# Kernel optimization log

Measured on AMD Instinct MI355X. Metric: run time of the kernel, lower is better.

## Reference

```python
import jax, jax.numpy as jnp
import numpy as np

B, T, C = 8, 2048, 1024
NEG = -1e30  # stand-in for -inf in the stable-softmax running max


def setup_inputs() -> dict:
    key = jax.random.key(0)
    ks = jax.random.split(key, 5)
    x = jax.random.normal(ks[0], (B, T, C), dtype=jnp.float32)
    scales = jnp.arange(C, dtype=jnp.float32) / C  # matches init_weight()
    Wk = jax.random.normal(ks[1], (C, C), dtype=jnp.float32) * 0.02
    Wv = jax.random.normal(ks[2], (C, C), dtype=jnp.float32) * 0.02
    Wr = jax.random.normal(ks[3], (C, C), dtype=jnp.float32) * 0.02
    Wo = jax.random.normal(ks[4], (C, C), dtype=jnp.float32) * 0.02
    return {
        'x': x,
        'w': scales, 'u': scales,
        'mix_k': scales, 'mix_v': scales, 'mix_r': scales,
        'Wk': Wk, 'Wv': Wv, 'Wr': Wr, 'Wo': Wo,
    }


def wkv(w, u, k, v):
    # Numerically-stable RWKV WKV recurrence. k, v: [B, T, C]; w, u: [C]
    w_exp = -jnp.exp(w)  # per-channel log-decay (negative)
    p0 = jnp.zeros(k.shape[::2], k.dtype)      # [B, C] numerator state
    q0 = jnp.zeros(k.shape[::2], k.dtype)      # [B, C] denominator state
    o0 = jnp.full(k.shape[::2], NEG, k.dtype)  # [B, C] running max (log-space)

    def step(carry, kv_t):
        p, q, o = carry
        k_t, v_t = kv_t  # each [B, C]
        uk = u + k_t
        no = jnp.maximum(o, uk)
        A = jnp.exp(o - no)
        Bc = jnp.exp(uk - no)
        out = (A * p + Bc * v_t) / (A * q + Bc)
        wo = w_exp + o
        no2 = jnp.maximum(wo, k_t)
        A2 = jnp.exp(wo - no2)
        B2 = jnp.exp(k_t - no2)
        return (A2 * p + B2 * v_t, A2 * q + B2, no2), out

    kT = jnp.swapaxes(k, 0, 1)  # [T, B, C]
    vT = jnp.swapaxes(v, 0, 1)
    _, outs = jax.lax.scan(step, (p0, q0, o0), (kT, vT))
    return jnp.swapaxes(outs, 0, 1)  # [B, T, C]


def reference(x, w, u, mix_k, mix_v, mix_r, Wk, Wv, Wr, Wo):
    # time_shift: ZeroPad2d((0,0,1,-1)) => shift sequence right by one, zero-pad front
    x_prev = jnp.pad(x, ((0, 0), (1, 0), (0, 0)))[:, :-1]
    # torch.lerp(start=x_prev, end=x, weight=mix)
    xk = x_prev + mix_k * (x - x_prev)
    xv = x_prev + mix_v * (x - x_prev)
    xr = x_prev + mix_r * (x - x_prev)
    k = jnp.einsum('btc,dc->btd', xk, Wk)
    v = jnp.einsum('btc,dc->btd', xv, Wv)
    sr = jax.nn.sigmoid(jnp.einsum('btc,dc->btd', xr, Wr))
    rwkv = sr * wkv(w, u, k, v)
    return jnp.einsum('btc,dc->btd', rwkv, Wo)
```

## Files before the change

### kernel.cpp

```cpp
#include <hip/hip_runtime.h>
#include <hip/hip_bf16.h>
#include <stdint.h>

#define Bb   8
#define Tt   2048
#define Cdim 1024
#define BT   16384
#define SLAB ((size_t)BT * Cdim)

#define NC   32
#define LCH  64
#define CSUB 32

typedef __attribute__((ext_vector_type(4))) float f32x4;
typedef __attribute__((ext_vector_type(8))) short bf16x8;

__device__ inline short f2bs(float f) {
    union { __hip_bfloat16 h; short s; } u;
    u.h = __float2bfloat16(f);
    return u.s;
}
__device__ inline float bs2f(short s) {
    union { short s; __hip_bfloat16 h; } u;
    u.s = s;
    return __bfloat162float(u.h);
}

#define GLOAD_LDS16(g, l) __builtin_amdgcn_global_load_lds( \
    (const __attribute__((address_space(1))) void*)(g),     \
    (__attribute__((address_space(3))) void*)(l), 16, 0, 0)

#define SBAR()      __builtin_amdgcn_s_barrier()

__global__ __launch_bounds__(256) void prep_all(
    const float* __restrict__ x,
    const float* __restrict__ mk,
    const float* __restrict__ mv,
    const float* __restrict__ mr,
    const float* __restrict__ Wk, const float* __restrict__ Wv,
    const float* __restrict__ Wr, const float* __restrict__ Wo,
    short* __restrict__ xmix,
    short* __restrict__ wbf)
{
    int bid = blockIdx.x;
    if (bid < 8192) {
        int idx = bid * 256 + threadIdx.x;
        int c8  = idx & (Cdim / 8 - 1);
        int m   = idx >> 7;
        int c0  = c8 << 3;
        int t   = m & (Tt - 1);

        float xs[8], ps[8];
        const float4* xp = (const float4*)(x + (size_t)m * Cdim + c0);
        float4 xa = xp[0], xb = xp[1];
        xs[0]=xa.x; xs[1]=xa.y; xs[2]=xa.z; xs[3]=xa.w;
        xs[4]=xb.x; xs[5]=xb.y; xs[6]=xb.z; xs[7]=xb.w;
        if (t != 0) {
            const float4* pp = (const float4*)(x + (size_t)(m - 1) * Cdim + c0);
            float4 pa = pp[0], pb = pp[1];
            ps[0]=pa.x; ps[1]=pa.y; ps[2]=pa.z; ps[3]=pa.w;
            ps[4]=pb.x; ps[5]=pb.y; ps[6]=pb.z; ps[7]=pb.w;
        } else {
            #pragma unroll
            for (int j = 0; j < 8; ++j) ps[j] = 0.f;
        }

        const float* mixes[3] = {mk, mv, mr};
        #pragma unroll
        for (int z = 0; z < 3; ++z) {
            const float4* mp = (const float4*)(mixes[z] + c0);
            float4 ma = mp[0], mb = mp[1];
            float mm[8];
            mm[0]=ma.x; mm[1]=ma.y; mm[2]=ma.z; mm[3]=ma.w;
            mm[4]=mb.x; mm[5]=mb.y; mm[6]=mb.z; mm[7]=mb.w;
            bf16x8 o;
            #pragma unroll
            for (int j = 0; j < 8; ++j)
                o[j] = f2bs(ps[j] + mm[j] * (xs[j] - ps[j]));
            *(bf16x8*)(xmix + (size_t)z * SLAB + (size_t)m * Cdim + c0) = o;
        }
    } else {
        int idx = (bid - 8192) * 256 + threadIdx.x;
        int z   = idx >> 17;
        int r   = idx & (Cdim * Cdim / 8 - 1);
        const float* src = (z == 0) ? Wk : (z == 1) ? Wv : (z == 2) ? Wr : Wo;
        const float4* sp = (const float4*)(src + (size_t)r * 8);
        float4 a = sp[0], b = sp[1];
        float v[8] = {a.x, a.y, a.z, a.w, b.x, b.y, b.z, b.w};
        bf16x8 o;
        #pragma unroll
        for (int j = 0; j < 8; ++j) o[j] = f2bs(v[j]);
        *(bf16x8*)(wbf + (size_t)z * Cdim * Cdim + (size_t)r * 8) = o;
    }
}

template<int FUSED>
__global__ __launch_bounds__(512, 2) void gemm256(
    const short* __restrict__ Abase,
    const short* __restrict__ Wbase,
    void* __restrict__ o0, void* __restrict__ o2)
{
    __shared__ __align__(16) char lds[131072];

    const int tid  = threadIdx.x;
    const int lane = tid & 63;
    const int wv   = tid >> 6;
    const int wm   = wv >> 2, wn = wv & 3;
    const int NT   = Cdim / 64;

    int orig = blockIdx.y * (FUSED ? 12 : 4) + blockIdx.x;
    int xcd  = orig & 7;
    int s    = orig >> 3;
    int z, nt, yt;
    if (FUSED) {
        if (s < 64) { int pr = s >> 1; z = s & 1; nt = pr & 3; yt = xcd * 8 + (pr >> 2); }
        else        { int rm = s - 64; z = 2;     nt = rm & 3; yt = xcd * 8 + (rm >> 2); }
    } else {
        z  = 0;
        nt = s & 3;
        yt = xcd * 8 + (s >> 2);
    }

    const short* A  = Abase + (size_t)z * SLAB;
    const short* Bm = Wbase + (size_t)z * Cdim * Cdim;
    const int m0 = yt * 256;
    const int n0 = nt * 256;

    f32x4 acc[8][4] = {};

    const int lm = lane & 15, lq = lane >> 4, lb7 = lane & 7;
    int ck[2];
    #pragma unroll
    for (int ks = 0; ks < 2; ++ks) ck[ks] = (((ks * 4 + lq) ^ lb7) << 4);
    int aoff[8];
    #pragma unroll
    for (int i = 0; i < 8; ++i) aoff[i] = (i * 16 + lm) * 128;
    int boff[4];
    #pragma unroll
    for (int j = 0; j < 4; ++j) boff[j] = ((wn & 1) * 64 + j * 16 + lm) * 128;
    const int aReg = wm << 14;
    const int bReg = 32768 + ((wn >> 1) << 14);

    const int rlo  = tid >> 3;
    const int clog = (tid & 7) ^ (rlo & 7);
    auto STAGE = [&](int tt, int part) {
        const short* mat = (part < 2) ? A : Bm;
        int rb = ((part < 2) ? m0 : n0) + ((part & 1) << 7);
        const short* g0 = mat + (size_t)(rb + rlo)      * Cdim + (tt << 6) + (clog << 3);
        const short* g1 = mat + (size_t)(rb + 64 + rlo) * Cdim + (tt << 6) + (clog << 3);
        char* l = lds + ((tt & 1) << 16) + (part << 14) + tid * 16;
        GLOAD_LDS16(g0, l);
        GLOAD_LDS16(g1, l + 8192);
    };

    STAGE(0, 0); STAGE(0, 1); STAGE(0, 2); STAGE(0, 3);
    asm volatile("s_waitcnt vmcnt(0)" ::: "memory");
    SBAR();

    bf16x8 a0[4][2], a4[4][2], b01[2][2], b23[2][2];

    #pragma unroll 1
    for (int kt = 0; kt < NT; ++kt) {
        const char* base = lds + ((kt & 1) << 16);

        #pragma unroll
        for (int i = 0; i < 4; ++i)
            #pragma unroll
            for (int ks = 0; ks < 2; ++ks)
                a0[i][ks] = *(const bf16x8*)(base + aReg + aoff[i] + ck[ks]);
        #pragma unroll
        for (int j = 0; j < 2; ++j)
            #pragma unroll
            for (int ks = 0; ks < 2; ++ks)
                b01[j][ks] = *(const bf16x8*)(base + bReg + boff[j] + ck[ks]);
        #pragma unroll
        for (int i = 0; i < 4; ++i)
            #pragma unroll
            for (int ks = 0; ks < 2; ++ks)
                a4[i][ks] = *(const bf16x8*)(base + aReg + aoff[i + 4] + ck[ks]);
        #pragma unroll
        for (int j = 0; j < 2; ++j)
            #pragma unroll
            for (int ks = 0; ks < 2; ++ks)
                b23[j][ks] = *(const bf16x8*)(base + bReg + boff[j + 2] + ck[ks]);

        if (kt + 1 < NT) {
            STAGE(kt + 1, 0); STAGE(kt + 1, 1);
            STAGE(kt + 1, 2); STAGE(kt + 1, 3);
        }

        #pragma unroll
        for (int ks = 0; ks < 2; ++ks)
            #pragma unroll
            for (int i = 0; i < 4; ++i)
                #pragma unroll
                for (int j = 0; j < 2; ++j)
                    acc[i][j] = __builtin_amdgcn_mfma_f32_16x16x32_bf16(
                        a0[i][ks], b01[j][ks], acc[i][j], 0, 0, 0);
        #pragma unroll
        for (int ks = 0; ks < 2; ++ks)
            #pragma unroll
            for (int i = 0; i < 4; ++i)
                #pragma unroll
                for (int j = 0; j < 2; ++j)
                    acc[i + 4][j] = __builtin_amdgcn_mfma_f32_16x16x32_bf16(
                        a4[i][ks], b01[j][ks], acc[i + 4][j], 0, 0, 0);
        #pragma unroll
        for (int ks = 0; ks < 2; ++ks)
            #pragma unroll
            for (int i = 0; i < 4; ++i)
                #pragma unroll
                for (int j = 0; j < 2; ++j)
                    acc[i + 4][j + 2] = __builtin_amdgcn_mfma_f32_16x16x32_bf16(
                        a4[i][ks], b23[j][ks], acc[i + 4][j + 2], 0, 0, 0);
        #pragma unroll
        for (int ks = 0; ks < 2; ++ks)
            #pragma unroll
            for (int i = 0; i < 4; ++i)
                #pragma unroll
                for (int j = 0; j < 2; ++j)
                    acc[i][j + 2] = __builtin_amdgcn_mfma_f32_16x16x32_bf16(
                        a0[i][ks], b23[j][ks], acc[i][j + 2], 0, 0, 0);

        if (kt + 1 < NT) {
            asm volatile("s_waitcnt vmcnt(0)" ::: "memory");
            SBAR();
        }
    }

    int col0 = n0 + wn * 64 + lm;
    int row0 = m0 + wm * 128 + (lq << 2);
    #pragma unroll
    for (int i = 0; i < 8; ++i) {
        #pragma unroll
        for (int j = 0; j < 4; ++j) {
            #pragma unroll
            for (int r = 0; r < 4; ++r) {
                int row = row0 + i * 16 + r;
                int cc  = col0 + j * 16;
                float vvv = acc[i][j][r];
                if (FUSED) {
                    if (z == 2) {
                        ((short*)o2)[(size_t)row * Cdim + cc] =
                            f2bs(1.f / (1.f + __expf(-vvv)));
                    } else {
                        ((short*)o0)[((size_t)row * Cdim + cc) * 2 + z] = f2bs(vvv);
                    }
                } else {
                    ((float*)o0)[(size_t)row * Cdim + cc] = vvv;
                }
            }
        }
    }
}

__global__ __launch_bounds__(1024) void wkv_chunked(
    const int* __restrict__ kv, const short* __restrict__ srb,
    const float* __restrict__ w, const float* __restrict__ u,
    short* __restrict__ rwkv)
{
    __shared__ float sp[NC][CSUB];
    __shared__ float sq[NC][CSUB];
    __shared__ float so[NC][CSUB];

    int tid = threadIdx.x;
    int cl  = tid & (CSUB - 1);
    int ch  = tid >> 5;
    int b   = blockIdx.x >> 5;
    int cg  = blockIdx.x & 31;
    int c   = cg * CSUB + cl;

    float wexp = -__expf(w[c]);
    float uu   = u[c];
    size_t coff = (size_t)b * Tt * Cdim + (size_t)(ch * LCH) * Cdim + c;

    float p = 0.f, q = 0.f, o = -1e30f;
    #pragma unroll 8
    for (int t = 0; t < LCH; ++t) {
        size_t off = coff + (size_t)t * Cdim;
        int pk = kv[off];
        float kt = bs2f((short)(pk & 0xffff));
        float vt = bs2f((short)((unsigned)pk >> 16));
        float wo  = wexp + o;
        float no  = fmaxf(wo, kt);
        float A   = __expf(wo - no);
        float B2  = __expf(kt - no);
        p = A * p + B2 * vt;
        q = A * q + B2;
        o = no;
    }
    sp[ch][cl] = p; sq[ch][cl] = q; so[ch][cl] = o;
    __syncthreads();

    if (tid < CSUB) {
        float Ld = wexp * (float)LCH;
        float cp = 0.f, cq = 0.f, co = -1e30f;
        for (int j = 0; j < NC; ++j) {
            float lp = sp[j][tid], lq = sq[j][tid], lo = so[j][tid];
            sp[j][tid] = cp; sq[j][tid] = cq; so[j][tid] = co;
            float od = co + Ld;
            float no = fmaxf(od, lo);
            float A  = __expf(od - no);
            float B2 = __expf(lo - no);
            cp = A * cp + B2 * lp;
            cq = A * cq + B2 * lq;
            co = no;
        }
    }
    __syncthreads();

    p = sp[ch][cl]; q = sq[ch][cl]; o = so[ch][cl];
    #pragma unroll 8
    for (int t = 0; t < LCH; ++t) {
        size_t off = coff + (size_t)t * Cdim;
        int pk = kv[off];
        float kt = bs2f((short)(pk & 0xffff));
        float vt = bs2f((short)((unsigned)pk >> 16));
        float sr = bs2f(srb[off]);

        float uk  = uu + kt;
        float no  = fmaxf(o, uk);
        float Aa  = __expf(o - no);
        float Bc  = __expf(uk - no);
        float out = (Aa * p + Bc * vt) / (Aa * q + Bc);

        float wo  = wexp + o;
        float no2 = fmaxf(wo, kt);
        float A2  = __expf(wo - no2);
        float B2  = __expf(kt - no2);
        p = A2 * p + B2 * vt;
        q = A2 * q + B2;
        o = no2;

        rwkv[off] = f2bs(sr * out);
    }
}

extern "C" void kernel_launch(void* const* d_in, const int* in_sizes, int n_in,
                              void* d_out, int out_size, void* d_ws, size_t ws_size,
                              hipStream_t stream)
{
    const float* x    = (const float*)d_in[0];
    const float* w    = (const float*)d_in[1];
    const float* u    = (const float*)d_in[2];
    const float* mixk = (const float*)d_in[3];
    const float* mixv = (const float*)d_in[4];
    const float* mixr = (const float*)d_in[5];
    const float* Wk   = (const float*)d_in[6];
    const float* Wv   = (const float*)d_in[7];
    const float* Wr   = (const float*)d_in[8];
    const float* Wo   = (const float*)d_in[9];

    char* ws = (char*)d_ws;
    short* xmix = (short*)ws;
    short* wbf  = (short*)(ws + 3 * SLAB * 2);
    short* rbuf = (short*)(ws + 3 * SLAB * 2 + (size_t)4 * Cdim * Cdim * 2);
    short* rwkv = (short*)ws;
    int*   kvbf = (int*)d_out;

    prep_all<<<8192 + 2048, 256, 0, stream>>>(x, mixk, mixv, mixr,
                                              Wk, Wv, Wr, Wo, xmix, wbf);

    dim3 gf(12, BT / 256);
    gemm256<1><<<gf, 512, 0, stream>>>(xmix, wbf, kvbf, rbuf);

    wkv_chunked<<<Bb * (Cdim / CSUB), 1024, 0, stream>>>(kvbf, rbuf, w, u, rwkv);

    dim3 go(Cdim / 256, BT / 256);
    gemm256<0><<<go, 512, 0, stream>>>(rwkv, wbf + 3 * (size_t)Cdim * Cdim,
                                       (float*)d_out, nullptr);
}
```

Before: 226.8 us.

## Replace fused 256-tile projection GEMM with simpler 128-tile kernel

The fused K/V/R projection GEMM moves from a 256x256 tile kernel with 512 threads and 128KB LDS to a new 128x128 tile kernel with 256 threads, 32KB LDS and a simple non-pipelined load/compute loop. The grid grows from 768 to 3072 blocks, which aims at better occupancy and load balance across CUs. The output GEMM is split into its own non-templated kernel. The trade-off is lower data reuse per tile and no overlap of global loads with MFMA work in the new kernel.

```diff
diff --git a/kernel.cpp b/kernel.cpp
--- a/kernel.cpp
+++ b/kernel.cpp
@@ -94,11 +94,113 @@
     }
 }
 
-template<int FUSED>
-__global__ __launch_bounds__(512, 2) void gemm256(
+__global__ __launch_bounds__(256) void gemm128(
     const short* __restrict__ Abase,
     const short* __restrict__ Wbase,
     void* __restrict__ o0, void* __restrict__ o2)
+{
+    __shared__ __align__(16) char lds[32768];
+
+    const int tid  = threadIdx.x;
+    const int lane = tid & 63;
+    const int wv   = tid >> 6;
+    const int wm   = wv >> 1, wn = wv & 1;
+    const int NT   = Cdim / 64;
+
+    int orig = blockIdx.y * 24 + blockIdx.x;
+    int xcd  = orig & 7;
+    int s    = orig >> 3;
+    int z, nt, yt;
+    if (s < 256) { int pr = s >> 1; z = s & 1; nt = pr & 7; yt = xcd * 16 + (pr >> 3); }
+    else         { int rm = s - 256; z = 2;     nt = rm & 7; yt = xcd * 16 + (rm >> 3); }
+
+    const short* A  = Abase + (size_t)z * SLAB;
+    const short* Bm = Wbase + (size_t)z * Cdim * Cdim;
+    const int m0 = yt * 128;
+    const int n0 = nt * 128;
+
+    f32x4 acc[4][4] = {};
+
+    const int lm = lane & 15, lq = lane >> 4, lb7 = lane & 7;
+    int ck[2];
+    #pragma unroll
+    for (int ks = 0; ks < 2; ++ks) ck[ks] = (((ks * 4 + lq) ^ lb7) << 4);
+    int aoff[4];
+    #pragma unroll
+    for (int i = 0; i < 4; ++i) aoff[i] = (wm * 64 + i * 16 + lm) * 128;
+    int boff[4];
+    #pragma unroll
+    for (int j = 0; j < 4; ++j) boff[j] = 16384 + (wn * 64 + j * 16 + lm) * 128;
+
+    const int rlo  = tid >> 3;
+    const int clog = (tid & 7) ^ (rlo & 7);
+    auto STAGE = [&](int tt, int part) {
+        const short* mat = (part < 2) ? A : Bm;
+        int rb = ((part < 2) ? m0 : n0) + ((part & 1) << 6);
+        const short* g0 = mat + (size_t)(rb + rlo)      * Cdim + (tt << 6) + (clog << 3);
+        const short* g1 = mat + (size_t)(rb + 32 + rlo) * Cdim + (tt << 6) + (clog << 3);
+        char* l = lds + (part << 13) + tid * 16;
+        GLOAD_LDS16(g0, l);
+        GLOAD_LDS16(g1, l + 4096);
+    };
+
+    bf16x8 af[4][2], bf[4][2];
+
+    #pragma unroll 1
+    for (int kt = 0; kt < NT; ++kt) {
+        STAGE(kt, 0); STAGE(kt, 1); STAGE(kt, 2); STAGE(kt, 3);
+        asm volatile("s_waitcnt vmcnt(0)" ::: "memory");
+        SBAR();
+
+        #pragma unroll
+        for (int i = 0; i < 4; ++i)
+            #pragma unroll
+            for (int ks = 0; ks < 2; ++ks)
+                af[i][ks] = *(const bf16x8*)(lds + aoff[i] + ck[ks]);
+        #pragma unroll
+        for (int j = 0; j < 4; ++j)
+            #pragma unroll
+            for (int ks = 0; ks < 2; ++ks)
+                bf[j][ks] = *(const bf16x8*)(lds + boff[j] + ck[ks]);
+
+        #pragma unroll
+        for (int ks = 0; ks < 2; ++ks)
+            #pragma unroll
+            for (int i = 0; i < 4; ++i)
+                #pragma unroll
+                for (int j = 0; j < 4; ++j)
+                    acc[i][j] = __builtin_amdgcn_mfma_f32_16x16x32_bf16(
+                        af[i][ks], bf[j][ks], acc[i][j], 0, 0, 0);
+
+        SBAR();
+    }
+
+    int col0 = n0 + wn * 64 + lm;
+    int row0 = m0 + wm * 64 + (lq << 2);
+    #pragma unroll
+    for (int i = 0; i < 4; ++i) {
+        #pragma unroll
+        for (int j = 0; j < 4; ++j) {
+            #pragma unroll
+            for (int r = 0; r < 4; ++r) {
+                int row = row0 + i * 16 + r;
+                int cc  = col0 + j * 16;
+                float vvv = acc[i][j][r];
+                if (z == 2) {
+                    ((short*)o2)[(size_t)row * Cdim + cc] =
+                        f2bs(1.f / (1.f + __expf(-vvv)));
+                } else {
+                    ((short*)o0)[((size_t)row * Cdim + cc) * 2 + z] = f2bs(vvv);
+                }
+            }
+        }
+    }
+}
+
+__global__ __launch_bounds__(512, 2) void gemm256o(
+    const short* __restrict__ A,
+    const short* __restrict__ Bm,
+    float* __restrict__ o0)
 {
     __shared__ __align__(16) char lds[131072];
 
@@ -108,21 +210,12 @@
     const int wm   = wv >> 2, wn = wv & 3;
     const int NT   = Cdim / 64;
 
-    int orig = blockIdx.y * (FUSED ? 12 : 4) + blockIdx.x;
+    int orig = blockIdx.y * 4 + blockIdx.x;
     int xcd  = orig & 7;
     int s    = orig >> 3;
-    int z, nt, yt;
-    if (FUSED) {
-        if (s < 64) { int pr = s >> 1; z = s & 1; nt = pr & 3; yt = xcd * 8 + (pr >> 2); }
-        else        { int rm = s - 64; z = 2;     nt = rm & 3; yt = xcd * 8 + (rm >> 2); }
-    } else {
-        z  = 0;
-        nt = s & 3;
-        yt = xcd * 8 + (s >> 2);
-    }
-
-    const short* A  = Abase + (size_t)z * SLAB;
-    const short* Bm = Wbase + (size_t)z * Cdim * Cdim;
+    int nt = s & 3;
+    int yt = xcd * 8 + (s >> 2);
+
     const int m0 = yt * 256;
     const int n0 = nt * 256;
 
@@ -231,27 +324,13 @@
     int col0 = n0 + wn * 64 + lm;
     int row0 = m0 + wm * 128 + (lq << 2);
     #pragma unroll
-    for (int i = 0; i < 8; ++i) {
-        #pragma unroll
-        for (int j = 0; j < 4; ++j) {
-            #pragma unroll
-            for (int r = 0; r < 4; ++r) {
-                int row = row0 + i * 16 + r;
-                int cc  = col0 + j * 16;
-                float vvv = acc[i][j][r];
-                if (FUSED) {
-                    if (z == 2) {
-                        ((short*)o2)[(size_t)row * Cdim + cc] =
-                            f2bs(1.f / (1.f + __expf(-vvv)));
-                    } else {
-                        ((short*)o0)[((size_t)row * Cdim + cc) * 2 + z] = f2bs(vvv);
-                    }
-                } else {
-                    ((float*)o0)[(size_t)row * Cdim + cc] = vvv;
-                }
-            }
-        }
-    }
+    for (int i = 0; i < 8; ++i)
+        #pragma unroll
+        for (int j = 0; j < 4; ++j)
+            #pragma unroll
+            for (int r = 0; r < 4; ++r)
+                o0[(size_t)(row0 + i * 16 + r) * Cdim + col0 + j * 16] =
+                    acc[i][j][r];
 }
 
 __global__ __launch_bounds__(1024) void wkv_chunked(
@@ -361,12 +440,12 @@
     prep_all<<<8192 + 2048, 256, 0, stream>>>(x, mixk, mixv, mixr,
                                               Wk, Wv, Wr, Wo, xmix, wbf);
 
-    dim3 gf(12, BT / 256);
-    gemm256<1><<<gf, 512, 0, stream>>>(xmix, wbf, kvbf, rbuf);
+    dim3 gf(24, 128);
+    gemm128<<<gf, 256, 0, stream>>>(xmix, wbf, kvbf, rbuf);
 
     wkv_chunked<<<Bb * (Cdim / CSUB), 1024, 0, stream>>>(kvbf, rbuf, w, u, rwkv);
 
     dim3 go(Cdim / 256, BT / 256);
-    gemm256<0><<<go, 512, 0, stream>>>(rwkv, wbf + 3 * (size_t)Cdim * Cdim,
-                                       (float*)d_out, nullptr);
-}
+    gemm256o<<<go, 512, 0, stream>>>(rwkv, wbf + 3 * (size_t)Cdim * Cdim,
+                                     (float*)d_out);
+}
```

Result: slower. 265.0 us (+16.9%).
